# Performance work log

Hardware: AMD Instinct MI355X
Metric: run time of the kernel (lower is better)

Reference implementation:

```python
import jax, jax.numpy as jnp
import numpy as np

N, T = 2048, 128
E, H = 128, 256
V, L = 30000, 1000


def setup_inputs() -> dict:
    key = jax.random.key(0)
    ks = jax.random.split(key, 10)
    tokens = jax.random.randint(ks[0], (N, T), 0, V)
    lengths = jax.random.randint(ks[1], (N,), 1, T + 1)  # each seq has >=1 valid step
    labels = jax.random.randint(ks[2], (N,), 0, L)
    s_e = 1.0 / np.sqrt(H)
    emb = jax.random.normal(ks[3], (V, E), dtype=jnp.float32)
    W_ih = jax.random.uniform(ks[4], (4 * H, E), minval=-s_e, maxval=s_e, dtype=jnp.float32)
    W_hh = jax.random.uniform(ks[5], (4 * H, H), minval=-s_e, maxval=s_e, dtype=jnp.float32)
    b_ih = jax.random.uniform(ks[6], (4 * H,), minval=-s_e, maxval=s_e, dtype=jnp.float32)
    b_hh = jax.random.uniform(ks[7], (4 * H,), minval=-s_e, maxval=s_e, dtype=jnp.float32)
    s_h = 1.0 / np.sqrt(H)
    W_out = jax.random.uniform(ks[8], (L, H), minval=-s_h, maxval=s_h, dtype=jnp.float32)
    b_out = jax.random.uniform(ks[9], (L,), minval=-s_h, maxval=s_h, dtype=jnp.float32)
    return {"tokens": tokens, "lengths": lengths, "labels": labels, "emb": emb,
            "W_ih": W_ih, "W_hh": W_hh, "b_ih": b_ih, "b_hh": b_hh,
            "W_out": W_out, "b_out": b_out}


def _lstm_final(tokens, lengths, emb, W_ih, W_hh, b_ih, b_hh):
    # Batched ragged LSTM: freeze state once t >= length (matches per-seq loop).
    x = emb[tokens]                                    # [N,T,E]
    xg = jnp.einsum('nte,ge->ntg', x, W_ih) + b_ih     # [N,T,4H] precomputed input gates
    xg_t = jnp.transpose(xg, (1, 0, 2))                # [T,N,4H]
    mask_t = (jnp.arange(T)[:, None] < lengths[None, :])  # [T,N]
    h0 = jnp.zeros((tokens.shape[0], H), jnp.float32)
    c0 = jnp.zeros_like(h0)

    def step(carry, inp):
        h, c = carry
        xgt, m = inp
        gates = xgt + h @ W_hh.T + b_hh                # [N,4H]
        i, f, g, o = jnp.split(gates, 4, axis=-1)
        i = jax.nn.sigmoid(i); f = jax.nn.sigmoid(f)
        g = jnp.tanh(g); o = jax.nn.sigmoid(o)
        c_new = f * c + i * g
        h_new = o * jnp.tanh(c_new)
        mm = m[:, None]
        return (jnp.where(mm, h_new, h), jnp.where(mm, c_new, c)), None

    (h_f, c_f), _ = jax.lax.scan(step, (h0, c0), (xg_t, mask_t))
    return h_f, c_f                                    # final valid h, c per sequence


def reference(tokens, lengths, labels, emb, W_ih, W_hh, b_ih, b_hh, W_out, b_out):
    h_f, c_f = _lstm_final(tokens, lengths, emb, W_ih, W_hh, b_ih, b_hh)
    logits = h_f @ W_out.T + b_out                     # [N,L]
    logp = jax.nn.log_softmax(logits, axis=-1)
    # NLLLoss per sequence, summed then divided by count -> mean
    loss = -jnp.mean(logp[jnp.arange(logp.shape[0]), labels])
    embeds = jnp.mean(c_f, axis=0)                     # mean of final cell states, [H]
    return embeds, loss
```

## Files before the change

### kernel.cpp

```cpp
#include <hip/hip_runtime.h>
#include <hip/hip_bf16.h>
#include <math.h>

#define NSEQ 2048
#define TT   128
#define EE   128
#define HH   256
#define GG   1024
#define LL   1000
#define NT   512
#define NGRP 32
#define NMEM 8
#define SEQG 64
#define NKT  12
#define NMT  64
#define NKT_O 8
#define WSA_ELEMS (NMT * NKT * 64 * 8)
#define WSO_ELEMS (NMT * NKT_O * 64 * 8)
#define GHF_SHORTS ((size_t)NGRP * NMEM * 2 * 4 * 64 * 8)

typedef __attribute__((ext_vector_type(8))) short bf16x8;
typedef __attribute__((ext_vector_type(4))) float f32x4;
typedef unsigned long long u64;

__device__ __forceinline__ unsigned short f2bf(float f) {
    union { float f; unsigned u; } v; v.f = f;
    unsigned r = v.u + 0x7FFF + ((v.u >> 16) & 1);
    return (unsigned short)(r >> 16);
}
__device__ __forceinline__ float sigf(float x) { return 1.0f / (1.0f + __expf(-x)); }
__device__ __forceinline__ float tanh_fast(float x) { return 1.0f - 2.0f / (1.0f + __expf(2.0f * x)); }

__device__ __forceinline__ void st8_sys(unsigned short* p, unsigned lo, unsigned hi) {
    u64 v = (u64)lo | ((u64)hi << 32);
    __hip_atomic_store((u64*)p, v, __ATOMIC_RELAXED, __HIP_MEMORY_SCOPE_SYSTEM);
}
__device__ __forceinline__ bf16x8 ld16_sys(const unsigned short* p) {
    u64 lo = __hip_atomic_load((const u64*)p,       __ATOMIC_RELAXED, __HIP_MEMORY_SCOPE_SYSTEM);
    u64 hi = __hip_atomic_load((const u64*)(p + 4), __ATOMIC_RELAXED, __HIP_MEMORY_SCOPE_SYSTEM);
    union { u64 q[2]; bf16x8 v; } u; u.q[0] = lo; u.q[1] = hi;
    return u.v;
}

__global__ void init_out_kernel(float* out, int* flags) {
    int i = blockIdx.x * blockDim.x + threadIdx.x;
    if (i < HH + 1) out[i] = 0.0f;
    if (i < NGRP * NMEM) flags[i] = 0;
}

__global__ void convert_weights(const float* __restrict__ Wih, const float* __restrict__ Whh,
                                const float* __restrict__ Wout,
                                unsigned short* __restrict__ wsA, unsigned short* __restrict__ wsO) {
    int gid = blockIdx.x * blockDim.x + threadIdx.x;
    if (gid < NMT * NKT * 64) {
        int lane = gid & 63, tile = gid >> 6;
        int kt = tile % NKT, mt = tile / NKT;
        int row = mt * 16 + (lane & 15);
        int kb  = kt * 32 + (lane >> 4) * 8;
        unsigned short o[8];
#pragma unroll
        for (int j = 0; j < 8; ++j) {
            int k = kb + j;
            float v = (k < EE) ? Wih[row * EE + k] : Whh[row * HH + (k - EE)];
            o[j] = f2bf(v);
        }
        uint4 pk;
        pk.x = o[0] | ((unsigned)o[1] << 16); pk.y = o[2] | ((unsigned)o[3] << 16);
        pk.z = o[4] | ((unsigned)o[5] << 16); pk.w = o[6] | ((unsigned)o[7] << 16);
        *(uint4*)(wsA + (size_t)gid * 8) = pk;
    } else {
        int g2 = gid - NMT * NKT * 64;
        if (g2 < NMT * NKT_O * 64) {
            int lane = g2 & 63, tile = g2 >> 6;
            int kt = tile % NKT_O, mt = tile / NKT_O;
            int row = mt * 16 + (lane & 15);
            int ub  = kt * 32 + (lane >> 4) * 8;
            unsigned short o[8];
#pragma unroll
            for (int j = 0; j < 8; ++j)
                o[j] = (row < LL) ? f2bf(Wout[row * HH + ub + j]) : (unsigned short)0;
            uint4 pk;
            pk.x = o[0] | ((unsigned)o[1] << 16); pk.y = o[2] | ((unsigned)o[3] << 16);
            pk.z = o[4] | ((unsigned)o[5] << 16); pk.w = o[6] | ((unsigned)o[7] << 16);
            *(uint4*)(wsO + (size_t)g2 * 8) = pk;
        }
    }
}

__launch_bounds__(NT, 2)
__global__ void lstm_group_kernel(
    const int* __restrict__ tokens, const int* __restrict__ lengths,
    const int* __restrict__ labels, const float* __restrict__ emb,
    const float* __restrict__ bih,  const float* __restrict__ bhh,
    const float* __restrict__ bout,
    const unsigned short* __restrict__ wsA, const unsigned short* __restrict__ wsO,
    unsigned short* __restrict__ ghf, int* __restrict__ flags,
    float* __restrict__ out)
{
    __shared__ __align__(16) unsigned short wlds[8 * 12 * 64 * 8];
    __shared__ __align__(16) unsigned short xfS[4 * 4 * 64 * 8];
    __shared__ __align__(16) unsigned short hf[2 * 4 * 64 * 8];
    __shared__ float redm[8][16];
    __shared__ float reds[8][16];
    __shared__ int   labv[SEQG];
    __shared__ int   ready_s;

    const int tid = threadIdx.x;
    const int w   = tid >> 6;
    const int l   = tid & 63;
    const int lq  = l >> 4;
    const int ls  = l & 15;
    const int jj  = w >> 2;
    const int cg  = w & 3;
    const int grp = blockIdx.x & (NGRP - 1);
    const int m   = blockIdx.x >> 5;
    const int n0  = grp * SEQG;

    int* const flagBase = flags + grp * NMEM;

    int maxlen = lengths[n0 + l];
#pragma unroll
    for (int s = 1; s < 64; s <<= 1) maxlen = max(maxlen, __shfl_xor(maxlen, s, 64));
    const int len_s = lengths[n0 + cg * 16 + ls];

    if (tid < SEQG) labv[tid] = labels[n0 + tid];
    if (tid == 0) ready_s = 0;

    f32x4 biasv[4];
#pragma unroll
    for (int g = 0; g < 4; ++g)
#pragma unroll
        for (int r = 0; r < 4; ++r) {
            int row = 256 * g + 32 * m + 16 * jj + 4 * lq + r;
            biasv[g][r] = bih[row] + bhh[row];
        }

    for (int idx = tid; idx < 8 * 12 * 64; idx += NT) {
        int mtl = idx / 768;
        int rem = idx - mtl * 768;
        int kt = rem >> 6, l2 = rem & 63;
        int g = mtl >> 1, j2 = mtl & 1;
        int gmt = 16 * g + 2 * m + j2;
        *(uint4*)&wlds[(size_t)idx * 8] =
            *(const uint4*)(wsA + ((size_t)(gmt * NKT + kt) * 64 + l2) * 8);
    }

    if (tid < 256) {
        uint4 z = {0, 0, 0, 0};
        *(uint4*)&hf[(size_t)tid * 8] = z;
        size_t base = ((size_t)((grp * NMEM + m) * 2 + 0) * 4) * 512 + (size_t)tid * 8;
        st8_sys(&ghf[base], 0, 0);
        st8_sys(&ghf[base + 4], 0, 0);
    }

    const int xs_s   = tid & 63;
    const int xs_oct = tid >> 6;

    auto stageX = [&](const f32x4* xv) {
#pragma unroll
        for (int dc = 0; dc < 4; ++dc) {
            int d0 = 16 * xs_oct + 4 * dc;
            int kt = d0 >> 5, cgs = xs_s >> 4;
            int lanep = (xs_s & 15) + 16 * ((d0 >> 3) & 3);
            uint2 pk;
            pk.x = f2bf(xv[dc][0]) | ((unsigned)f2bf(xv[dc][1]) << 16);
            pk.y = f2bf(xv[dc][2]) | ((unsigned)f2bf(xv[dc][3]) << 16);
            *(uint2*)&xfS[(size_t)((kt * 4 + cgs) * 64 + lanep) * 8 + (d0 & 4)] = pk;
        }
    };

    {
        int tok = tokens[(n0 + xs_s) * TT + 0];
        const float* er = emb + (size_t)tok * EE + 16 * xs_oct;
        f32x4 x0[4];
#pragma unroll
        for (int dc = 0; dc < 4; ++dc) x0[dc] = *(const f32x4*)(er + 4 * dc);
        stageX(x0);
    }
    __syncthreads();
    if (tid == 0)
        __hip_atomic_store(&flagBase[m], 1, __ATOMIC_RELAXED, __HIP_MEMORY_SCOPE_SYSTEM);

    f32x4 xv[4];
    if (maxlen > 1) {
        int tok = tokens[(n0 + xs_s) * TT + 1];
        const float* er = emb + (size_t)tok * EE + 16 * xs_oct;
#pragma unroll
        for (int dc = 0; dc < 4; ++dc) xv[dc] = *(const f32x4*)(er + 4 * dc);
    }

    f32x4 acc[4], accN[4];
#pragma unroll
    for (int g = 0; g < 4; ++g) acc[g] = biasv[g];
#pragma unroll
    for (int kt = 0; kt < 4; ++kt) {
        const bf16x8 bx = *(const bf16x8*)&xfS[(size_t)((kt * 4 + cg) * 64 + l) * 8];
#pragma unroll
        for (int g = 0; g < 4; ++g)
            acc[g] = __builtin_amdgcn_mfma_f32_16x16x32_bf16(
                *(const bf16x8*)&wlds[(size_t)(((2 * g + jj) * 12 + kt) * 64 + l) * 8],
                bx, acc[g], 0, 0, 0);
    }
    __syncthreads();

    auto relay_wait = [&](int need) {
        if (w == 0) {
            int f;
            do {
                f = 0x7fffffff;
                if (l < NMEM)
                    f = __hip_atomic_load(&flagBase[l], __ATOMIC_RELAXED, __HIP_MEMORY_SCOPE_SYSTEM);
                f = min(f, __shfl_xor(f, 1, 64));
                f = min(f, __shfl_xor(f, 2, 64));
                f = min(f, __shfl_xor(f, 4, 64));
                f = __shfl(f, 0, 64);
                if (f < need) __builtin_amdgcn_s_sleep(2);
            } while (f < need);
            __hip_atomic_store(&ready_s, need, __ATOMIC_RELEASE, __HIP_MEMORY_SCOPE_WORKGROUP);
        } else {
            while (__hip_atomic_load(&ready_s, __ATOMIC_ACQUIRE, __HIP_MEMORY_SCOPE_WORKGROUP) < need)
                __builtin_amdgcn_s_sleep(1);
        }
    };

    float c_reg[4], h_reg[4];
#pragma unroll
    for (int r = 0; r < 4; ++r) { c_reg[r] = 0.0f; h_reg[r] = 0.0f; }

    const int u8      = 2 * jj + (lq >> 1);
    const int lanep_h = 16 * u8 + ls;
    const int joff_h  = 4 * (lq & 1);
    const size_t gb0  = ((size_t)((grp * NMEM + m) * 2 + 0) * 4 + cg) * 512 + (size_t)lanep_h * 8 + joff_h;
    const size_t gb1  = gb0 + 4 * 512;

    for (int t = 0; t < maxlen; ++t) {
        const int cur = t & 1, nxt = cur ^ 1;
        const bool doX = (t + 1 < maxlen);

        if (doX) stageX(xv);
        const bf16x8 bo = *(const bf16x8*)&hf[(size_t)((cur * 4 + cg) * 64 + l) * 8];
        if (doX) __syncthreads();

        if (t + 2 < maxlen) {
            int tok = tokens[(n0 + xs_s) * TT + t + 2];
            const float* er = emb + (size_t)tok * EE + 16 * xs_oct;
#pragma unroll
            for (int dc = 0; dc < 4; ++dc) xv[dc] = *(const f32x4*)(er + 4 * dc);
        }

        if (doX) {
#pragma unroll
            for (int g = 0; g < 4; ++g) accN[g] = biasv[g];
#pragma unroll
            for (int kt = 0; kt < 4; ++kt) {
                const bf16x8 bx = *(const bf16x8*)&xfS[(size_t)((kt * 4 + cg) * 64 + l) * 8];
#pragma unroll
                for (int g = 0; g < 4; ++g)
                    accN[g] = __builtin_amdgcn_mfma_f32_16x16x32_bf16(
                        *(const bf16x8*)&wlds[(size_t)(((2 * g + jj) * 12 + kt) * 64 + l) * 8],
                        bx, accN[g], 0, 0, 0);
            }
        }

        relay_wait(t + 1);

        bf16x8 bp[7];
#pragma unroll
        for (int i = 0; i < 7; ++i) {
            int p = i + (i >= m ? 1 : 0);
            size_t b = ((size_t)((grp * NMEM + p) * 2 + cur) * 4 + cg) * 512;
            bp[i] = ld16_sys(&ghf[b + (size_t)l * 8]);
        }

#pragma unroll
        for (int g = 0; g < 4; ++g)
            acc[g] = __builtin_amdgcn_mfma_f32_16x16x32_bf16(
                *(const bf16x8*)&wlds[(size_t)(((2 * g + jj) * 12 + 4 + m) * 64 + l) * 8],
                bo, acc[g], 0, 0, 0);
#pragma unroll
        for (int i = 0; i < 7; ++i) {
            int p = i + (i >= m ? 1 : 0);
            int kt = 4 + p;
#pragma unroll
            for (int g = 0; g < 4; ++g)
                acc[g] = __builtin_amdgcn_mfma_f32_16x16x32_bf16(
                    *(const bf16x8*)&wlds[(size_t)(((2 * g + jj) * 12 + kt) * 64 + l) * 8],
                    bp[i], acc[g], 0, 0, 0);
        }

        const bool live = (t < len_s);
#pragma unroll
        for (int r = 0; r < 4; ++r) {
            if (live) {
                float ig = sigf(acc[0][r]);
                float fg = sigf(acc[1][r]);
                float gg = tanh_fast(acc[2][r]);
                float og = sigf(acc[3][r]);
                float cc = fg * c_reg[r] + ig * gg;
                c_reg[r] = cc;
                h_reg[r] = og * tanh_fast(cc);
            }
        }

        if (doX) {
#pragma unroll
            for (int g = 0; g < 4; ++g) acc[g] = accN[g];
        }

        {
            uint2 hp;
            hp.x = f2bf(h_reg[0]) | ((unsigned)f2bf(h_reg[1]) << 16);
            hp.y = f2bf(h_reg[2]) | ((unsigned)f2bf(h_reg[3]) << 16);
            *(uint2*)&hf[(size_t)((nxt * 4 + cg) * 64 + lanep_h) * 8 + joff_h] = hp;
            st8_sys(&ghf[((t + 1) & 1) ? gb1 : gb0], hp.x, hp.y);
        }

        __syncthreads();
        if (tid == 0)
            __hip_atomic_store(&flagBase[m], t + 2, __ATOMIC_RELAXED, __HIP_MEMORY_SCOPE_SYSTEM);
    }

#pragma unroll
    for (int r = 0; r < 4; ++r) {
        float v = c_reg[r];
        v += __shfl_xor(v, 1, 64);
        v += __shfl_xor(v, 2, 64);
        v += __shfl_xor(v, 4, 64);
        v += __shfl_xor(v, 8, 64);
        if (ls == 0)
            atomicAdd(&out[32 * m + 16 * jj + 4 * lq + r], v * (1.0f / NSEQ));
    }

    if (m == 0) {
        relay_wait(maxlen + 1);
        const int fin = maxlen & 1;
        float* lg = (float*)wlds;
        float lossAcc = 0.0f;

        for (int cgo = 0; cgo < 4; ++cgo) {
            bf16x8 bq[8];
#pragma unroll
            for (int p = 0; p < 8; ++p) {
                size_t b = ((size_t)((grp * NMEM + p) * 2 + fin) * 4 + cgo) * 512;
                bq[p] = ld16_sys(&ghf[b + (size_t)l * 8]);
            }
            __syncthreads();
#pragma unroll
            for (int i = 0; i < 8; ++i) {
                int mt = 8 * w + i;
                f32x4 a = {0.0f, 0.0f, 0.0f, 0.0f};
#pragma unroll
                for (int p = 0; p < 8; ++p)
                    a = __builtin_amdgcn_mfma_f32_16x16x32_bf16(
                        *(const bf16x8*)(wsO + ((size_t)(mt * NKT_O + p) * 64 + l) * 8),
                        bq[p], a, 0, 0, 0);
#pragma unroll
                for (int r = 0; r < 4; ++r) {
                    int cls = 16 * mt + 4 * lq + r;
                    lg[(size_t)ls * 1024 + cls] = (cls < LL) ? (a[r] + bout[cls]) : -INFINITY;
                }
            }
            __syncthreads();
            const int s2 = tid >> 5;
            const int i2 = tid & 31;
            const float* row = &lg[(size_t)s2 * 1024];
            float mx = -INFINITY;
#pragma unroll
            for (int k = 0; k < 32; ++k) mx = fmaxf(mx, row[i2 + 32 * k]);
            mx = fmaxf(mx, __shfl_xor(mx, 1, 64));
            mx = fmaxf(mx, __shfl_xor(mx, 2, 64));
            mx = fmaxf(mx, __shfl_xor(mx, 4, 64));
            mx = fmaxf(mx, __shfl_xor(mx, 8, 64));
            mx = fmaxf(mx, __shfl_xor(mx, 16, 64));
            float sm = 0.0f;
#pragma unroll
            for (int k = 0; k < 32; ++k) sm += __expf(row[i2 + 32 * k] - mx);
            sm += __shfl_xor(sm, 1, 64);
            sm += __shfl_xor(sm, 2, 64);
            sm += __shfl_xor(sm, 4, 64);
            sm += __shfl_xor(sm, 8, 64);
            sm += __shfl_xor(sm, 16, 64);
            if (i2 == 0) {
                int lab = labv[cgo * 16 + s2];
                float lp = row[lab] - mx - __logf(sm);
                lossAcc += -lp;
            }
        }
        if ((tid & 31) == 0)
            atomicAdd(&out[HH], lossAcc * (1.0f / NSEQ));
    }
}

extern "C" void kernel_launch(void* const* d_in, const int* in_sizes, int n_in,
                              void* d_out, int out_size, void* d_ws, size_t ws_size,
                              hipStream_t stream)
{
    const int*   tokens  = (const int*)d_in[0];
    const int*   lengths = (const int*)d_in[1];
    const int*   labels  = (const int*)d_in[2];
    const float* emb     = (const float*)d_in[3];
    const float* Wih     = (const float*)d_in[4];
    const float* Whh     = (const float*)d_in[5];
    const float* bih     = (const float*)d_in[6];
    const float* bhh     = (const float*)d_in[7];
    const float* Wout    = (const float*)d_in[8];
    const float* bout    = (const float*)d_in[9];
    float* out = (float*)d_out;

    unsigned short* wsA  = (unsigned short*)d_ws;
    unsigned short* wsO  = wsA + WSA_ELEMS;
    unsigned short* ghf  = wsO + WSO_ELEMS;
    int*            flg  = (int*)(ghf + GHF_SHORTS);

    hipLaunchKernelGGL(init_out_kernel, dim3(1), dim3(512), 0, stream, out, flg);
    {
        int nthr = NMT * NKT * 64 + NMT * NKT_O * 64;
        hipLaunchKernelGGL(convert_weights, dim3((nthr + 255) / 256), dim3(256), 0, stream,
                           Wih, Whh, Wout, wsA, wsO);
    }
    hipLaunchKernelGGL(lstm_group_kernel, dim3(NGRP * NMEM), dim3(NT), 0, stream,
                       tokens, lengths, labels, emb, bih, bhh, bout, wsA, wsO, ghf, flg, out);
}
```

Measured before the change: 698.9 us.

## Replace block-wide barriers with per-wave flags and per-column-group step counts

Each wave now publishes its own progress flag and waits only on the eight member blocks' flags for its own 16-sequence column group, so the per-step __syncthreads and the wave-0 relay are gone. Each wave gathers and stages its own embedding slice in a private LDS region, and each column group runs only to the max length of its 16 sequences rather than the whole 64-sequence group. Own-block hidden state is now read back through global memory instead of LDS. This cuts intra-block barrier stalls and wasted steps on short groups, at the price of more flag traffic and extra polling by every wave.

```diff
diff --git a/kernel.cpp b/kernel.cpp
--- a/kernel.cpp
+++ b/kernel.cpp
@@ -18,6 +18,7 @@
 #define WSA_ELEMS (NMT * NKT * 64 * 8)
 #define WSO_ELEMS (NMT * NKT_O * 64 * 8)
 #define GHF_SHORTS ((size_t)NGRP * NMEM * 2 * 4 * 64 * 8)
+#define NFLAGS (NGRP * NMEM * 8)
 
 typedef __attribute__((ext_vector_type(8))) short bf16x8;
 typedef __attribute__((ext_vector_type(4))) float f32x4;
@@ -45,7 +46,7 @@
 __global__ void init_out_kernel(float* out, int* flags) {
     int i = blockIdx.x * blockDim.x + threadIdx.x;
     if (i < HH + 1) out[i] = 0.0f;
-    if (i < NGRP * NMEM) flags[i] = 0;
+    if (i < NFLAGS) flags[i] = 0;
 }
 
 __global__ void convert_weights(const float* __restrict__ Wih, const float* __restrict__ Whh,
@@ -98,12 +99,9 @@
     float* __restrict__ out)
 {
     __shared__ __align__(16) unsigned short wlds[8 * 12 * 64 * 8];
-    __shared__ __align__(16) unsigned short xfS[4 * 4 * 64 * 8];
-    __shared__ __align__(16) unsigned short hf[2 * 4 * 64 * 8];
-    __shared__ float redm[8][16];
-    __shared__ float reds[8][16];
-    __shared__ int   labv[SEQG];
-    __shared__ int   ready_s;
+    __shared__ __align__(16) unsigned short xf[8 * 4 * 64 * 8];
+    __shared__ int labv[SEQG];
+    __shared__ int mxl[4];
 
     const int tid = threadIdx.x;
     const int w   = tid >> 6;
@@ -116,15 +114,15 @@
     const int m   = blockIdx.x >> 5;
     const int n0  = grp * SEQG;
 
-    int* const flagBase = flags + grp * NMEM;
-
-    int maxlen = lengths[n0 + l];
-#pragma unroll
-    for (int s = 1; s < 64; s <<= 1) maxlen = max(maxlen, __shfl_xor(maxlen, s, 64));
+    int* const flagBase = flags + grp * (NMEM * 8);
+
+    int mg = lengths[n0 + l];
+#pragma unroll
+    for (int s = 1; s < 16; s <<= 1) mg = max(mg, __shfl_xor(mg, s, 64));
+    const int maxlen_c = __shfl(mg, cg * 16, 64);
     const int len_s = lengths[n0 + cg * 16 + ls];
-
+    if (w == 0 && ls == 0) mxl[lq] = mg;
     if (tid < SEQG) labv[tid] = labels[n0 + tid];
-    if (tid == 0) ready_s = 0;
 
     f32x4 biasv[4];
 #pragma unroll
@@ -144,88 +142,7 @@
         *(uint4*)&wlds[(size_t)idx * 8] =
             *(const uint4*)(wsA + ((size_t)(gmt * NKT + kt) * 64 + l2) * 8);
     }
-
-    if (tid < 256) {
-        uint4 z = {0, 0, 0, 0};
-        *(uint4*)&hf[(size_t)tid * 8] = z;
-        size_t base = ((size_t)((grp * NMEM + m) * 2 + 0) * 4) * 512 + (size_t)tid * 8;
-        st8_sys(&ghf[base], 0, 0);
-        st8_sys(&ghf[base + 4], 0, 0);
-    }
-
-    const int xs_s   = tid & 63;
-    const int xs_oct = tid >> 6;
-
-    auto stageX = [&](const f32x4* xv) {
-#pragma unroll
-        for (int dc = 0; dc < 4; ++dc) {
-            int d0 = 16 * xs_oct + 4 * dc;
-            int kt = d0 >> 5, cgs = xs_s >> 4;
-            int lanep = (xs_s & 15) + 16 * ((d0 >> 3) & 3);
-            uint2 pk;
-            pk.x = f2bf(xv[dc][0]) | ((unsigned)f2bf(xv[dc][1]) << 16);
-            pk.y = f2bf(xv[dc][2]) | ((unsigned)f2bf(xv[dc][3]) << 16);
-            *(uint2*)&xfS[(size_t)((kt * 4 + cgs) * 64 + lanep) * 8 + (d0 & 4)] = pk;
-        }
-    };
-
-    {
-        int tok = tokens[(n0 + xs_s) * TT + 0];
-        const float* er = emb + (size_t)tok * EE + 16 * xs_oct;
-        f32x4 x0[4];
-#pragma unroll
-        for (int dc = 0; dc < 4; ++dc) x0[dc] = *(const f32x4*)(er + 4 * dc);
-        stageX(x0);
-    }
     __syncthreads();
-    if (tid == 0)
-        __hip_atomic_store(&flagBase[m], 1, __ATOMIC_RELAXED, __HIP_MEMORY_SCOPE_SYSTEM);
-
-    f32x4 xv[4];
-    if (maxlen > 1) {
-        int tok = tokens[(n0 + xs_s) * TT + 1];
-        const float* er = emb + (size_t)tok * EE + 16 * xs_oct;
-#pragma unroll
-        for (int dc = 0; dc < 4; ++dc) xv[dc] = *(const f32x4*)(er + 4 * dc);
-    }
-
-    f32x4 acc[4], accN[4];
-#pragma unroll
-    for (int g = 0; g < 4; ++g) acc[g] = biasv[g];
-#pragma unroll
-    for (int kt = 0; kt < 4; ++kt) {
-        const bf16x8 bx = *(const bf16x8*)&xfS[(size_t)((kt * 4 + cg) * 64 + l) * 8];
-#pragma unroll
-        for (int g = 0; g < 4; ++g)
-            acc[g] = __builtin_amdgcn_mfma_f32_16x16x32_bf16(
-                *(const bf16x8*)&wlds[(size_t)(((2 * g + jj) * 12 + kt) * 64 + l) * 8],
-                bx, acc[g], 0, 0, 0);
-    }
-    __syncthreads();
-
-    auto relay_wait = [&](int need) {
-        if (w == 0) {
-            int f;
-            do {
-                f = 0x7fffffff;
-                if (l < NMEM)
-                    f = __hip_atomic_load(&flagBase[l], __ATOMIC_RELAXED, __HIP_MEMORY_SCOPE_SYSTEM);
-                f = min(f, __shfl_xor(f, 1, 64));
-                f = min(f, __shfl_xor(f, 2, 64));
-                f = min(f, __shfl_xor(f, 4, 64));
-                f = __shfl(f, 0, 64);
-                if (f < need) __builtin_amdgcn_s_sleep(2);
-            } while (f < need);
-            __hip_atomic_store(&ready_s, need, __ATOMIC_RELEASE, __HIP_MEMORY_SCOPE_WORKGROUP);
-        } else {
-            while (__hip_atomic_load(&ready_s, __ATOMIC_ACQUIRE, __HIP_MEMORY_SCOPE_WORKGROUP) < need)
-                __builtin_amdgcn_s_sleep(1);
-        }
-    };
-
-    float c_reg[4], h_reg[4];
-#pragma unroll
-    for (int r = 0; r < 4; ++r) { c_reg[r] = 0.0f; h_reg[r] = 0.0f; }
 
     const int u8      = 2 * jj + (lq >> 1);
     const int lanep_h = 16 * u8 + ls;
@@ -233,19 +150,85 @@
     const size_t gb0  = ((size_t)((grp * NMEM + m) * 2 + 0) * 4 + cg) * 512 + (size_t)lanep_h * 8 + joff_h;
     const size_t gb1  = gb0 + 4 * 512;
 
-    for (int t = 0; t < maxlen; ++t) {
-        const int cur = t & 1, nxt = cur ^ 1;
-        const bool doX = (t + 1 < maxlen);
-
-        if (doX) stageX(xv);
-        const bf16x8 bo = *(const bf16x8*)&hf[(size_t)((cur * 4 + cg) * 64 + l) * 8];
-        if (doX) __syncthreads();
-
-        if (t + 2 < maxlen) {
-            int tok = tokens[(n0 + xs_s) * TT + t + 2];
-            const float* er = emb + (size_t)tok * EE + 16 * xs_oct;
-#pragma unroll
-            for (int dc = 0; dc < 4; ++dc) xv[dc] = *(const f32x4*)(er + 4 * dc);
+    st8_sys(&ghf[gb0], 0u, 0u);
+    asm volatile("s_waitcnt vmcnt(0)" ::: "memory");
+    if (l == 0)
+        __hip_atomic_store(&flagBase[m * 8 + w], 1, __ATOMIC_RELAXED, __HIP_MEMORY_SCOPE_SYSTEM);
+
+    const int q = lq;
+    unsigned short* const xfw = xf + (size_t)w * (4 * 64 * 8);
+    const int seqi = (n0 + cg * 16 + ls) * TT;
+
+    f32x4 xg[8];
+    auto gatherX = [&](int t) {
+        int tok = tokens[seqi + t];
+        const float* er = emb + (size_t)tok * EE + 32 * q;
+#pragma unroll
+        for (int j2 = 0; j2 < 8; ++j2) xg[j2] = *(const f32x4*)(er + 4 * j2);
+    };
+    auto stageX = [&]() {
+#pragma unroll
+        for (int dcp = 0; dcp < 4; ++dcp) {
+            uint4 pk;
+            pk.x = f2bf(xg[2*dcp][0])   | ((unsigned)f2bf(xg[2*dcp][1])   << 16);
+            pk.y = f2bf(xg[2*dcp][2])   | ((unsigned)f2bf(xg[2*dcp][3])   << 16);
+            pk.z = f2bf(xg[2*dcp+1][0]) | ((unsigned)f2bf(xg[2*dcp+1][1]) << 16);
+            pk.w = f2bf(xg[2*dcp+1][2]) | ((unsigned)f2bf(xg[2*dcp+1][3]) << 16);
+            *(uint4*)&xfw[(size_t)(q * 64 + ls + 16 * dcp) * 8] = pk;
+        }
+    };
+
+    gatherX(0);
+    stageX();
+    if (maxlen_c > 1) gatherX(1);
+
+    f32x4 acc[4], accN[4];
+#pragma unroll
+    for (int g = 0; g < 4; ++g) acc[g] = biasv[g];
+#pragma unroll
+    for (int kt = 0; kt < 4; ++kt) {
+        const bf16x8 bx = *(const bf16x8*)&xfw[(size_t)(kt * 64 + l) * 8];
+#pragma unroll
+        for (int g = 0; g < 4; ++g)
+            acc[g] = __builtin_amdgcn_mfma_f32_16x16x32_bf16(
+                *(const bf16x8*)&wlds[(size_t)(((2 * g + jj) * 12 + kt) * 64 + l) * 8],
+                bx, acc[g], 0, 0, 0);
+    }
+
+    float c_reg[4], h_reg[4];
+#pragma unroll
+    for (int r = 0; r < 4; ++r) { c_reg[r] = 0.0f; h_reg[r] = 0.0f; }
+
+    for (int t = 0; t < maxlen_c; ++t) {
+        const int cur = t & 1;
+        const bool doX = (t + 1 < maxlen_c);
+
+        if (doX) stageX();
+        if (t + 2 < maxlen_c) gatherX(t + 2);
+
+        bf16x8 bp[8];
+        {
+            const int need = t + 1;
+            unsigned loaded = 0;
+            do {
+                int fa = 0x7fffffff;
+                if (l < 8) {
+                    int f0 = __hip_atomic_load(&flagBase[l * 8 + cg],     __ATOMIC_RELAXED, __HIP_MEMORY_SCOPE_SYSTEM);
+                    int f1 = __hip_atomic_load(&flagBase[l * 8 + cg + 4], __ATOMIC_RELAXED, __HIP_MEMORY_SCOPE_SYSTEM);
+                    fa = min(f0, f1);
+                }
+                unsigned rm = (unsigned)__ballot(fa >= need) & 0xFFu;
+                unsigned newp = rm & ~loaded;
+                if (newp) {
+#pragma unroll
+                    for (int p = 0; p < 8; ++p)
+                        if (newp & (1u << p)) {
+                            size_t b = ((size_t)((grp * NMEM + p) * 2 + cur) * 4 + cg) * 512;
+                            bp[p] = ld16_sys(&ghf[b + (size_t)l * 8]);
+                        }
+                    loaded |= newp;
+                }
+            } while (loaded != 0xFFu);
         }
 
         if (doX) {
@@ -253,7 +236,7 @@
             for (int g = 0; g < 4; ++g) accN[g] = biasv[g];
 #pragma unroll
             for (int kt = 0; kt < 4; ++kt) {
-                const bf16x8 bx = *(const bf16x8*)&xfS[(size_t)((kt * 4 + cg) * 64 + l) * 8];
+                const bf16x8 bx = *(const bf16x8*)&xfw[(size_t)(kt * 64 + l) * 8];
 #pragma unroll
                 for (int g = 0; g < 4; ++g)
                     accN[g] = __builtin_amdgcn_mfma_f32_16x16x32_bf16(
@@ -262,31 +245,13 @@
             }
         }
 
-        relay_wait(t + 1);
-
-        bf16x8 bp[7];
-#pragma unroll
-        for (int i = 0; i < 7; ++i) {
-            int p = i + (i >= m ? 1 : 0);
-            size_t b = ((size_t)((grp * NMEM + p) * 2 + cur) * 4 + cg) * 512;
-            bp[i] = ld16_sys(&ghf[b + (size_t)l * 8]);
-        }
-
-#pragma unroll
-        for (int g = 0; g < 4; ++g)
-            acc[g] = __builtin_amdgcn_mfma_f32_16x16x32_bf16(
-                *(const bf16x8*)&wlds[(size_t)(((2 * g + jj) * 12 + 4 + m) * 64 + l) * 8],
-                bo, acc[g], 0, 0, 0);
-#pragma unroll
-        for (int i = 0; i < 7; ++i) {
-            int p = i + (i >= m ? 1 : 0);
-            int kt = 4 + p;
+#pragma unroll
+        for (int p = 0; p < 8; ++p)
 #pragma unroll
             for (int g = 0; g < 4; ++g)
                 acc[g] = __builtin_amdgcn_mfma_f32_16x16x32_bf16(
-                    *(const bf16x8*)&wlds[(size_t)(((2 * g + jj) * 12 + kt) * 64 + l) * 8],
-                    bp[i], acc[g], 0, 0, 0);
-        }
+                    *(const bf16x8*)&wlds[(size_t)(((2 * g + jj) * 12 + 4 + p) * 64 + l) * 8],
+                    bp[p], acc[g], 0, 0, 0);
 
         const bool live = (t < len_s);
 #pragma unroll
@@ -302,22 +267,20 @@
             }
         }
 
-        if (doX) {
-#pragma unroll
-            for (int g = 0; g < 4; ++g) acc[g] = accN[g];
-        }
-
         {
             uint2 hp;
             hp.x = f2bf(h_reg[0]) | ((unsigned)f2bf(h_reg[1]) << 16);
             hp.y = f2bf(h_reg[2]) | ((unsigned)f2bf(h_reg[3]) << 16);
-            *(uint2*)&hf[(size_t)((nxt * 4 + cg) * 64 + lanep_h) * 8 + joff_h] = hp;
-            st8_sys(&ghf[((t + 1) & 1) ? gb1 : gb0], hp.x, hp.y);
-        }
-
-        __syncthreads();
-        if (tid == 0)
-            __hip_atomic_store(&flagBase[m], t + 2, __ATOMIC_RELAXED, __HIP_MEMORY_SCOPE_SYSTEM);
+            st8_sys(&ghf[(t & 1) ? gb0 : gb1], hp.x, hp.y);
+        }
+        asm volatile("s_waitcnt vmcnt(0)" ::: "memory");
+        if (l == 0)
+            __hip_atomic_store(&flagBase[m * 8 + w], t + 2, __ATOMIC_RELAXED, __HIP_MEMORY_SCOPE_SYSTEM);
+
+        if (doX) {
+#pragma unroll
+            for (int g = 0; g < 4; ++g) acc[g] = accN[g];
+        }
     }
 
 #pragma unroll
@@ -332,12 +295,24 @@
     }
 
     if (m == 0) {
-        relay_wait(maxlen + 1);
-        const int fin = maxlen & 1;
+        {
+            const int p_ = l >> 3, w_ = l & 7;
+            const int tgt = mxl[w_ & 3] + 1;
+            int d;
+            do {
+                int f = __hip_atomic_load(&flagBase[p_ * 8 + w_], __ATOMIC_RELAXED, __HIP_MEMORY_SCOPE_SYSTEM);
+                d = f - tgt;
+#pragma unroll
+                for (int s = 1; s < 64; s <<= 1) d = min(d, __shfl_xor(d, s, 64));
+                if (d < 0) __builtin_amdgcn_s_sleep(2);
+            } while (d < 0);
+        }
+
         float* lg = (float*)wlds;
         float lossAcc = 0.0f;
 
         for (int cgo = 0; cgo < 4; ++cgo) {
+            const int fin = mxl[cgo] & 1;
             bf16x8 bq[8];
 #pragma unroll
             for (int p = 0; p < 8; ++p) {
@@ -412,7 +387,7 @@
     unsigned short* ghf  = wsO + WSO_ELEMS;
     int*            flg  = (int*)(ghf + GHF_SHORTS);
 
-    hipLaunchKernelGGL(init_out_kernel, dim3(1), dim3(512), 0, stream, out, flg);
+    hipLaunchKernelGGL(init_out_kernel, dim3(4), dim3(512), 0, stream, out, flg);
     {
         int nthr = NMT * NKT * 64 + NMT * NKT_O * 64;
         hipLaunchKernelGGL(convert_weights, dim3((nthr + 255) / 256), dim3(256), 0, stream,
```

After: 1.533 ms. +119.3%, slower.

## Use agent-scope atomics for h relay when group blocks share an XCD

Applied to the files above, without the earlier changes.

Each block records its XCC id at startup. After the first flag barrier, a group checks whether all 8 member blocks landed on the same XCD; if so, the per-step hidden-state exchange and flag polling use agent-scope atomics instead of system-scope ones. The aim is to cut the latency of the cross-block recurrent handoff. Correctness then relies on agent scope being coherent within one XCD, and the fast path only helps when the scheduler happens to co-locate a group's blocks on the same XCD, which the default blockIdx mapping (grp = blockIdx & 31, m = blockIdx >> 5) may rarely do.

```diff
diff --git a/kernel.cpp b/kernel.cpp
--- a/kernel.cpp
+++ b/kernel.cpp
@@ -18,6 +18,7 @@
 #define WSA_ELEMS (NMT * NKT * 64 * 8)
 #define WSO_ELEMS (NMT * NKT_O * 64 * 8)
 #define GHF_SHORTS ((size_t)NGRP * NMEM * 2 * 4 * 64 * 8)
+#define XCD_OFF (NGRP * NMEM)
 
 typedef __attribute__((ext_vector_type(8))) short bf16x8;
 typedef __attribute__((ext_vector_type(4))) float f32x4;
@@ -31,21 +32,36 @@
 __device__ __forceinline__ float sigf(float x) { return 1.0f / (1.0f + __expf(-x)); }
 __device__ __forceinline__ float tanh_fast(float x) { return 1.0f - 2.0f / (1.0f + __expf(2.0f * x)); }
 
-__device__ __forceinline__ void st8_sys(unsigned short* p, unsigned lo, unsigned hi) {
+__device__ __forceinline__ void st8(unsigned short* p, unsigned lo, unsigned hi, bool fast) {
     u64 v = (u64)lo | ((u64)hi << 32);
-    __hip_atomic_store((u64*)p, v, __ATOMIC_RELAXED, __HIP_MEMORY_SCOPE_SYSTEM);
-}
-__device__ __forceinline__ bf16x8 ld16_sys(const unsigned short* p) {
-    u64 lo = __hip_atomic_load((const u64*)p,       __ATOMIC_RELAXED, __HIP_MEMORY_SCOPE_SYSTEM);
-    u64 hi = __hip_atomic_load((const u64*)(p + 4), __ATOMIC_RELAXED, __HIP_MEMORY_SCOPE_SYSTEM);
+    if (fast) __hip_atomic_store((u64*)p, v, __ATOMIC_RELAXED, __HIP_MEMORY_SCOPE_AGENT);
+    else      __hip_atomic_store((u64*)p, v, __ATOMIC_RELAXED, __HIP_MEMORY_SCOPE_SYSTEM);
+}
+__device__ __forceinline__ bf16x8 ld16(const unsigned short* p, bool fast) {
+    u64 lo, hi;
+    if (fast) {
+        lo = __hip_atomic_load((const u64*)p,       __ATOMIC_RELAXED, __HIP_MEMORY_SCOPE_AGENT);
+        hi = __hip_atomic_load((const u64*)(p + 4), __ATOMIC_RELAXED, __HIP_MEMORY_SCOPE_AGENT);
+    } else {
+        lo = __hip_atomic_load((const u64*)p,       __ATOMIC_RELAXED, __HIP_MEMORY_SCOPE_SYSTEM);
+        hi = __hip_atomic_load((const u64*)(p + 4), __ATOMIC_RELAXED, __HIP_MEMORY_SCOPE_SYSTEM);
+    }
     union { u64 q[2]; bf16x8 v; } u; u.q[0] = lo; u.q[1] = hi;
     return u.v;
+}
+__device__ __forceinline__ int ld_flag(const int* p, bool fast) {
+    if (fast) return __hip_atomic_load(p, __ATOMIC_RELAXED, __HIP_MEMORY_SCOPE_AGENT);
+    return __hip_atomic_load(p, __ATOMIC_RELAXED, __HIP_MEMORY_SCOPE_SYSTEM);
+}
+__device__ __forceinline__ void st_flag(int* p, int v, bool fast) {
+    if (fast) __hip_atomic_store(p, v, __ATOMIC_RELAXED, __HIP_MEMORY_SCOPE_AGENT);
+    else      __hip_atomic_store(p, v, __ATOMIC_RELAXED, __HIP_MEMORY_SCOPE_SYSTEM);
 }
 
 __global__ void init_out_kernel(float* out, int* flags) {
     int i = blockIdx.x * blockDim.x + threadIdx.x;
     if (i < HH + 1) out[i] = 0.0f;
-    if (i < NGRP * NMEM) flags[i] = 0;
+    if (i < 2 * NGRP * NMEM) flags[i] = 0;
 }
 
 __global__ void convert_weights(const float* __restrict__ Wih, const float* __restrict__ Whh,
@@ -100,8 +116,6 @@
     __shared__ __align__(16) unsigned short wlds[8 * 12 * 64 * 8];
     __shared__ __align__(16) unsigned short xfS[4 * 4 * 64 * 8];
     __shared__ __align__(16) unsigned short hf[2 * 4 * 64 * 8];
-    __shared__ float redm[8][16];
-    __shared__ float reds[8][16];
     __shared__ int   labv[SEQG];
     __shared__ int   ready_s;
 
@@ -117,6 +131,7 @@
     const int n0  = grp * SEQG;
 
     int* const flagBase = flags + grp * NMEM;
+    int* const xcdBase  = flags + XCD_OFF + grp * NMEM;
 
     int maxlen = lengths[n0 + l];
 #pragma unroll
@@ -145,12 +160,20 @@
             *(const uint4*)(wsA + ((size_t)(gmt * NKT + kt) * 64 + l2) * 8);
     }
 
+    {
+        unsigned xcc;
+        asm volatile("s_getreg_b32 %0, hwreg(HW_REG_XCC_ID)" : "=s"(xcc));
+        if (tid == 0)
+            __hip_atomic_store(&xcdBase[m], (int)(xcc + 1),
+                               __ATOMIC_RELAXED, __HIP_MEMORY_SCOPE_SYSTEM);
+    }
+
     if (tid < 256) {
         uint4 z = {0, 0, 0, 0};
         *(uint4*)&hf[(size_t)tid * 8] = z;
         size_t base = ((size_t)((grp * NMEM + m) * 2 + 0) * 4) * 512 + (size_t)tid * 8;
-        st8_sys(&ghf[base], 0, 0);
-        st8_sys(&ghf[base + 4], 0, 0);
+        st8(&ghf[base], 0, 0, false);
+        st8(&ghf[base + 4], 0, 0, false);
     }
 
     const int xs_s   = tid & 63;
@@ -181,35 +204,13 @@
     if (tid == 0)
         __hip_atomic_store(&flagBase[m], 1, __ATOMIC_RELAXED, __HIP_MEMORY_SCOPE_SYSTEM);
 
-    f32x4 xv[4];
-    if (maxlen > 1) {
-        int tok = tokens[(n0 + xs_s) * TT + 1];
-        const float* er = emb + (size_t)tok * EE + 16 * xs_oct;
-#pragma unroll
-        for (int dc = 0; dc < 4; ++dc) xv[dc] = *(const f32x4*)(er + 4 * dc);
-    }
-
-    f32x4 acc[4], accN[4];
-#pragma unroll
-    for (int g = 0; g < 4; ++g) acc[g] = biasv[g];
-#pragma unroll
-    for (int kt = 0; kt < 4; ++kt) {
-        const bf16x8 bx = *(const bf16x8*)&xfS[(size_t)((kt * 4 + cg) * 64 + l) * 8];
-#pragma unroll
-        for (int g = 0; g < 4; ++g)
-            acc[g] = __builtin_amdgcn_mfma_f32_16x16x32_bf16(
-                *(const bf16x8*)&wlds[(size_t)(((2 * g + jj) * 12 + kt) * 64 + l) * 8],
-                bx, acc[g], 0, 0, 0);
-    }
-    __syncthreads();
-
-    auto relay_wait = [&](int need) {
+    auto relay_wait = [&](int need, bool fastm) {
         if (w == 0) {
             int f;
             do {
                 f = 0x7fffffff;
                 if (l < NMEM)
-                    f = __hip_atomic_load(&flagBase[l], __ATOMIC_RELAXED, __HIP_MEMORY_SCOPE_SYSTEM);
+                    f = ld_flag(&flagBase[l], fastm);
                 f = min(f, __shfl_xor(f, 1, 64));
                 f = min(f, __shfl_xor(f, 2, 64));
                 f = min(f, __shfl_xor(f, 4, 64));
@@ -223,6 +224,38 @@
         }
     };
 
+    relay_wait(1, false);
+    bool fast;
+    {
+        int x = (l < NMEM)
+            ? __hip_atomic_load(&xcdBase[l], __ATOMIC_RELAXED, __HIP_MEMORY_SCOPE_SYSTEM) : 0;
+        int x0 = __shfl(x, 0, 64);
+        bool eq = (l >= NMEM) || (x == x0 && x != 0);
+        fast = (__ballot(eq) == ~0ull);
+    }
+
+    f32x4 xv[4];
+    if (maxlen > 1) {
+        int tok = tokens[(n0 + xs_s) * TT + 1];
+        const float* er = emb + (size_t)tok * EE + 16 * xs_oct;
+#pragma unroll
+        for (int dc = 0; dc < 4; ++dc) xv[dc] = *(const f32x4*)(er + 4 * dc);
+    }
+
+    f32x4 acc[4], accN[4];
+#pragma unroll
+    for (int g = 0; g < 4; ++g) acc[g] = biasv[g];
+#pragma unroll
+    for (int kt = 0; kt < 4; ++kt) {
+        const bf16x8 bx = *(const bf16x8*)&xfS[(size_t)((kt * 4 + cg) * 64 + l) * 8];
+#pragma unroll
+        for (int g = 0; g < 4; ++g)
+            acc[g] = __builtin_amdgcn_mfma_f32_16x16x32_bf16(
+                *(const bf16x8*)&wlds[(size_t)(((2 * g + jj) * 12 + kt) * 64 + l) * 8],
+                bx, acc[g], 0, 0, 0);
+    }
+    __syncthreads();
+
     float c_reg[4], h_reg[4];
 #pragma unroll
     for (int r = 0; r < 4; ++r) { c_reg[r] = 0.0f; h_reg[r] = 0.0f; }
@@ -262,14 +295,14 @@
             }
         }
 
-        relay_wait(t + 1);
+        relay_wait(t + 1, fast);
 
         bf16x8 bp[7];
 #pragma unroll
         for (int i = 0; i < 7; ++i) {
             int p = i + (i >= m ? 1 : 0);
             size_t b = ((size_t)((grp * NMEM + p) * 2 + cur) * 4 + cg) * 512;
-            bp[i] = ld16_sys(&ghf[b + (size_t)l * 8]);
+            bp[i] = ld16(&ghf[b + (size_t)l * 8], fast);
         }
 
 #pragma unroll
@@ -312,12 +345,12 @@
             hp.x = f2bf(h_reg[0]) | ((unsigned)f2bf(h_reg[1]) << 16);
             hp.y = f2bf(h_reg[2]) | ((unsigned)f2bf(h_reg[3]) << 16);
             *(uint2*)&hf[(size_t)((nxt * 4 + cg) * 64 + lanep_h) * 8 + joff_h] = hp;
-            st8_sys(&ghf[((t + 1) & 1) ? gb1 : gb0], hp.x, hp.y);
+            st8(&ghf[((t + 1) & 1) ? gb1 : gb0], hp.x, hp.y, fast);
         }
 
         __syncthreads();
         if (tid == 0)
-            __hip_atomic_store(&flagBase[m], t + 2, __ATOMIC_RELAXED, __HIP_MEMORY_SCOPE_SYSTEM);
+            st_flag(&flagBase[m], t + 2, fast);
     }
 
 #pragma unroll
@@ -332,7 +365,7 @@
     }
 
     if (m == 0) {
-        relay_wait(maxlen + 1);
+        relay_wait(maxlen + 1, fast);
         const int fin = maxlen & 1;
         float* lg = (float*)wlds;
         float lossAcc = 0.0f;
@@ -342,7 +375,7 @@
 #pragma unroll
             for (int p = 0; p < 8; ++p) {
                 size_t b = ((size_t)((grp * NMEM + p) * 2 + fin) * 4 + cgo) * 512;
-                bq[p] = ld16_sys(&ghf[b + (size_t)l * 8]);
+                bq[p] = ld16(&ghf[b + (size_t)l * 8], fast);
             }
             __syncthreads();
 #pragma unroll
```

Measured after the change: 737.7 us. 1.06x slower.

## Use XCD-local cached loads/stores for inter-block relay when group shares an XCD

Applied to the files above, without the earlier changes.

Each block publishes its XCC id, and the group checks whether all 8 member blocks run on the same XCD. If they do, the per-step h exchange and flag polling switch from system-scope atomics to plain global stores and sc0 loads that stay coherent within the XCD's L2, and the polling loop drops its sleep. The seven neighbour h loads are also issued back to back before a single wait. This is meant to cut cross-block synchronisation latency on every timestep, but it depends on the hardware scheduler co-locating blocks (block ids strided by 32 across 8 XCDs), and it relies on inline asm memory semantics.

```diff
diff --git a/kernel.cpp b/kernel.cpp
--- a/kernel.cpp
+++ b/kernel.cpp
@@ -18,9 +18,13 @@
 #define WSA_ELEMS (NMT * NKT * 64 * 8)
 #define WSO_ELEMS (NMT * NKT_O * 64 * 8)
 #define GHF_SHORTS ((size_t)NGRP * NMEM * 2 * 4 * 64 * 8)
+#define FLG_STRIDE 32
+#define XCD_OFF (NGRP * FLG_STRIDE)
+#define NFLAGW  (2 * NGRP * FLG_STRIDE)
 
 typedef __attribute__((ext_vector_type(8))) short bf16x8;
 typedef __attribute__((ext_vector_type(4))) float f32x4;
+typedef __attribute__((ext_vector_type(4))) unsigned int u32x4;
 typedef unsigned long long u64;
 
 __device__ __forceinline__ unsigned short f2bf(float f) {
@@ -42,10 +46,30 @@
     return u.v;
 }
 
+__device__ __forceinline__ void st8_f(unsigned short* p, unsigned lo, unsigned hi) {
+    u64 v = (u64)lo | ((u64)hi << 32);
+    asm volatile("global_store_dwordx2 %0, %1, off" :: "v"(p), "v"(v) : "memory");
+}
+__device__ __forceinline__ void stflag_f(int* p, int v) {
+    asm volatile("global_store_dword %0, %1, off" :: "v"(p), "v"(v) : "memory");
+}
+__device__ __forceinline__ int ldflag_f(const int* p) {
+    int r;
+    asm volatile("global_load_dword %0, %1, off sc0\n\t"
+                 "s_waitcnt vmcnt(0)" : "=v"(r) : "v"(p) : "memory");
+    return r;
+}
+__device__ __forceinline__ bf16x8 ld16_f(const unsigned short* p) {
+    union { u32x4 q; bf16x8 v; } u;
+    asm volatile("global_load_dwordx4 %0, %1, off sc0\n\t"
+                 "s_waitcnt vmcnt(0)" : "=v"(u.q) : "v"(p) : "memory");
+    return u.v;
+}
+
 __global__ void init_out_kernel(float* out, int* flags) {
     int i = blockIdx.x * blockDim.x + threadIdx.x;
     if (i < HH + 1) out[i] = 0.0f;
-    if (i < NGRP * NMEM) flags[i] = 0;
+    if (i < NFLAGW) flags[i] = 0;
 }
 
 __global__ void convert_weights(const float* __restrict__ Wih, const float* __restrict__ Whh,
@@ -100,10 +124,9 @@
     __shared__ __align__(16) unsigned short wlds[8 * 12 * 64 * 8];
     __shared__ __align__(16) unsigned short xfS[4 * 4 * 64 * 8];
     __shared__ __align__(16) unsigned short hf[2 * 4 * 64 * 8];
-    __shared__ float redm[8][16];
-    __shared__ float reds[8][16];
     __shared__ int   labv[SEQG];
     __shared__ int   ready_s;
+    __shared__ int   fast_s;
 
     const int tid = threadIdx.x;
     const int w   = tid >> 6;
@@ -116,7 +139,8 @@
     const int m   = blockIdx.x >> 5;
     const int n0  = grp * SEQG;
 
-    int* const flagBase = flags + grp * NMEM;
+    int* const flagBase = flags + grp * FLG_STRIDE;
+    int* const xcdBase  = flags + XCD_OFF + grp * FLG_STRIDE;
 
     int maxlen = lengths[n0 + l];
 #pragma unroll
@@ -124,7 +148,7 @@
     const int len_s = lengths[n0 + cg * 16 + ls];
 
     if (tid < SEQG) labv[tid] = labels[n0 + tid];
-    if (tid == 0) ready_s = 0;
+    if (tid == 0) { ready_s = 0; fast_s = 0; }
 
     f32x4 biasv[4];
 #pragma unroll
@@ -134,6 +158,14 @@
             int row = 256 * g + 32 * m + 16 * jj + 4 * lq + r;
             biasv[g][r] = bih[row] + bhh[row];
         }
+
+    {
+        unsigned xcc;
+        asm volatile("s_getreg_b32 %0, hwreg(HW_REG_XCC_ID)" : "=s"(xcc));
+        if (tid == 0)
+            __hip_atomic_store(&xcdBase[m], (int)(xcc + 1),
+                               __ATOMIC_RELAXED, __HIP_MEMORY_SCOPE_SYSTEM);
+    }
 
     for (int idx = tid; idx < 8 * 12 * 64; idx += NT) {
         int mtl = idx / 768;
@@ -145,14 +177,6 @@
             *(const uint4*)(wsA + ((size_t)(gmt * NKT + kt) * 64 + l2) * 8);
     }
 
-    if (tid < 256) {
-        uint4 z = {0, 0, 0, 0};
-        *(uint4*)&hf[(size_t)tid * 8] = z;
-        size_t base = ((size_t)((grp * NMEM + m) * 2 + 0) * 4) * 512 + (size_t)tid * 8;
-        st8_sys(&ghf[base], 0, 0);
-        st8_sys(&ghf[base + 4], 0, 0);
-    }
-
     const int xs_s   = tid & 63;
     const int xs_oct = tid >> 6;
 
@@ -177,44 +201,49 @@
         for (int dc = 0; dc < 4; ++dc) x0[dc] = *(const f32x4*)(er + 4 * dc);
         stageX(x0);
     }
+
+    if (w == 0) {
+        int x;
+        for (;;) {
+            x = (l < NMEM)
+                ? __hip_atomic_load(&xcdBase[l], __ATOMIC_RELAXED, __HIP_MEMORY_SCOPE_SYSTEM)
+                : 1;
+            if (__ballot(x != 0) == ~0ull) break;
+            __builtin_amdgcn_s_sleep(2);
+        }
+        int x0 = __shfl(x, 0, 64);
+        bool eq = (l >= NMEM) || (x == x0);
+        if (l == 0) fast_s = (__ballot(eq) == ~0ull) ? 1 : 0;
+    }
     __syncthreads();
-    if (tid == 0)
-        __hip_atomic_store(&flagBase[m], 1, __ATOMIC_RELAXED, __HIP_MEMORY_SCOPE_SYSTEM);
-
-    f32x4 xv[4];
-    if (maxlen > 1) {
-        int tok = tokens[(n0 + xs_s) * TT + 1];
-        const float* er = emb + (size_t)tok * EE + 16 * xs_oct;
-#pragma unroll
-        for (int dc = 0; dc < 4; ++dc) xv[dc] = *(const f32x4*)(er + 4 * dc);
-    }
-
-    f32x4 acc[4], accN[4];
-#pragma unroll
-    for (int g = 0; g < 4; ++g) acc[g] = biasv[g];
-#pragma unroll
-    for (int kt = 0; kt < 4; ++kt) {
-        const bf16x8 bx = *(const bf16x8*)&xfS[(size_t)((kt * 4 + cg) * 64 + l) * 8];
-#pragma unroll
-        for (int g = 0; g < 4; ++g)
-            acc[g] = __builtin_amdgcn_mfma_f32_16x16x32_bf16(
-                *(const bf16x8*)&wlds[(size_t)(((2 * g + jj) * 12 + kt) * 64 + l) * 8],
-                bx, acc[g], 0, 0, 0);
+    const bool fast = (fast_s != 0);
+
+    if (tid < 256) {
+        uint4 z = {0, 0, 0, 0};
+        *(uint4*)&hf[(size_t)tid * 8] = z;
+        size_t base = ((size_t)((grp * NMEM + m) * 2 + 0) * 4) * 512 + (size_t)tid * 8;
+        if (fast) { st8_f(&ghf[base], 0, 0);   st8_f(&ghf[base + 4], 0, 0); }
+        else      { st8_sys(&ghf[base], 0, 0); st8_sys(&ghf[base + 4], 0, 0); }
     }
     __syncthreads();
-
-    auto relay_wait = [&](int need) {
+    if (tid == 0) {
+        if (fast) stflag_f(&flagBase[m], 1);
+        else      __hip_atomic_store(&flagBase[m], 1, __ATOMIC_RELAXED, __HIP_MEMORY_SCOPE_SYSTEM);
+    }
+
+    auto relay_wait = [&](int need, bool fm) {
         if (w == 0) {
             int f;
             do {
                 f = 0x7fffffff;
                 if (l < NMEM)
-                    f = __hip_atomic_load(&flagBase[l], __ATOMIC_RELAXED, __HIP_MEMORY_SCOPE_SYSTEM);
+                    f = fm ? ldflag_f(&flagBase[l])
+                           : __hip_atomic_load(&flagBase[l], __ATOMIC_RELAXED, __HIP_MEMORY_SCOPE_SYSTEM);
                 f = min(f, __shfl_xor(f, 1, 64));
                 f = min(f, __shfl_xor(f, 2, 64));
                 f = min(f, __shfl_xor(f, 4, 64));
                 f = __shfl(f, 0, 64);
-                if (f < need) __builtin_amdgcn_s_sleep(2);
+                if (f < need && !fm) __builtin_amdgcn_s_sleep(2);
             } while (f < need);
             __hip_atomic_store(&ready_s, need, __ATOMIC_RELEASE, __HIP_MEMORY_SCOPE_WORKGROUP);
         } else {
@@ -223,6 +252,28 @@
         }
     };
 
+    f32x4 xv[4];
+    if (maxlen > 1) {
+        int tok = tokens[(n0 + xs_s) * TT + 1];
+        const float* er = emb + (size_t)tok * EE + 16 * xs_oct;
+#pragma unroll
+        for (int dc = 0; dc < 4; ++dc) xv[dc] = *(const f32x4*)(er + 4 * dc);
+    }
+
+    f32x4 acc[4], accN[4];
+#pragma unroll
+    for (int g = 0; g < 4; ++g) acc[g] = biasv[g];
+#pragma unroll
+    for (int kt = 0; kt < 4; ++kt) {
+        const bf16x8 bx = *(const bf16x8*)&xfS[(size_t)((kt * 4 + cg) * 64 + l) * 8];
+#pragma unroll
+        for (int g = 0; g < 4; ++g)
+            acc[g] = __builtin_amdgcn_mfma_f32_16x16x32_bf16(
+                *(const bf16x8*)&wlds[(size_t)(((2 * g + jj) * 12 + kt) * 64 + l) * 8],
+                bx, acc[g], 0, 0, 0);
+    }
+    __syncthreads();
+
     float c_reg[4], h_reg[4];
 #pragma unroll
     for (int r = 0; r < 4; ++r) { c_reg[r] = 0.0f; h_reg[r] = 0.0f; }
@@ -262,14 +313,36 @@
             }
         }
 
-        relay_wait(t + 1);
+        relay_wait(t + 1, fast);
 
         bf16x8 bp[7];
-#pragma unroll
-        for (int i = 0; i < 7; ++i) {
-            int p = i + (i >= m ? 1 : 0);
-            size_t b = ((size_t)((grp * NMEM + p) * 2 + cur) * 4 + cg) * 512;
-            bp[i] = ld16_sys(&ghf[b + (size_t)l * 8]);
+        if (fast) {
+            const unsigned short* pa[7];
+#pragma unroll
+            for (int i = 0; i < 7; ++i) {
+                int p = i + (i >= m ? 1 : 0);
+                size_t b = ((size_t)((grp * NMEM + p) * 2 + cur) * 4 + cg) * 512;
+                pa[i] = &ghf[b + (size_t)l * 8];
+            }
+            union { u32x4 q; bf16x8 v; } u0, u1, u2, u3, u4, u5, u6;
+            asm volatile("global_load_dwordx4 %0, %1, off sc0" : "=v"(u0.q) : "v"(pa[0]) : "memory");
+            asm volatile("global_load_dwordx4 %0, %1, off sc0" : "=v"(u1.q) : "v"(pa[1]) : "memory");
+            asm volatile("global_load_dwordx4 %0, %1, off sc0" : "=v"(u2.q) : "v"(pa[2]) : "memory");
+            asm volatile("global_load_dwordx4 %0, %1, off sc0" : "=v"(u3.q) : "v"(pa[3]) : "memory");
+            asm volatile("global_load_dwordx4 %0, %1, off sc0" : "=v"(u4.q) : "v"(pa[4]) : "memory");
+            asm volatile("global_load_dwordx4 %0, %1, off sc0" : "=v"(u5.q) : "v"(pa[5]) : "memory");
+            asm volatile("global_load_dwordx4 %0, %1, off sc0" : "=v"(u6.q) : "v"(pa[6]) : "memory");
+            asm volatile("s_waitcnt vmcnt(0)" ::: "memory");
+            __builtin_amdgcn_sched_barrier(0);
+            bp[0] = u0.v; bp[1] = u1.v; bp[2] = u2.v; bp[3] = u3.v;
+            bp[4] = u4.v; bp[5] = u5.v; bp[6] = u6.v;
+        } else {
+#pragma unroll
+            for (int i = 0; i < 7; ++i) {
+                int p = i + (i >= m ? 1 : 0);
+                size_t b = ((size_t)((grp * NMEM + p) * 2 + cur) * 4 + cg) * 512;
+                bp[i] = ld16_sys(&ghf[b + (size_t)l * 8]);
+            }
         }
 
 #pragma unroll
@@ -312,12 +385,16 @@
             hp.x = f2bf(h_reg[0]) | ((unsigned)f2bf(h_reg[1]) << 16);
             hp.y = f2bf(h_reg[2]) | ((unsigned)f2bf(h_reg[3]) << 16);
             *(uint2*)&hf[(size_t)((nxt * 4 + cg) * 64 + lanep_h) * 8 + joff_h] = hp;
-            st8_sys(&ghf[((t + 1) & 1) ? gb1 : gb0], hp.x, hp.y);
+            unsigned short* gp = &ghf[((t + 1) & 1) ? gb1 : gb0];
+            if (fast) st8_f(gp, hp.x, hp.y);
+            else      st8_sys(gp, hp.x, hp.y);
         }
 
         __syncthreads();
-        if (tid == 0)
-            __hip_atomic_store(&flagBase[m], t + 2, __ATOMIC_RELAXED, __HIP_MEMORY_SCOPE_SYSTEM);
+        if (tid == 0) {
+            if (fast) stflag_f(&flagBase[m], t + 2);
+            else      __hip_atomic_store(&flagBase[m], t + 2, __ATOMIC_RELAXED, __HIP_MEMORY_SCOPE_SYSTEM);
+        }
     }
 
 #pragma unroll
@@ -332,7 +409,7 @@
     }
 
     if (m == 0) {
-        relay_wait(maxlen + 1);
+        relay_wait(maxlen + 1, fast);
         const int fin = maxlen & 1;
         float* lg = (float*)wlds;
         float lossAcc = 0.0f;
@@ -342,7 +419,8 @@
 #pragma unroll
             for (int p = 0; p < 8; ++p) {
                 size_t b = ((size_t)((grp * NMEM + p) * 2 + fin) * 4 + cgo) * 512;
-                bq[p] = ld16_sys(&ghf[b + (size_t)l * 8]);
+                const unsigned short* ptr = &ghf[b + (size_t)l * 8];
+                bq[p] = fast ? ld16_f(ptr) : ld16_sys(ptr);
             }
             __syncthreads();
 #pragma unroll
@@ -412,7 +490,7 @@
     unsigned short* ghf  = wsO + WSO_ELEMS;
     int*            flg  = (int*)(ghf + GHF_SHORTS);
 
-    hipLaunchKernelGGL(init_out_kernel, dim3(1), dim3(512), 0, stream, out, flg);
+    hipLaunchKernelGGL(init_out_kernel, dim3(4), dim3(512), 0, stream, out, flg);
     {
         int nthr = NMT * NKT * 64 + NMT * NKT_O * 64;
         hipLaunchKernelGGL(convert_weights, dim3((nthr + 255) / 256), dim3(256), 0, stream,
```

After: 727.4 us. +4.1%, slower.
